# Optimization experiments

Hardware: AMD Instinct MI355X
Metric: run time of the kernel (lower is better)

Reference implementation:

```python
import jax, jax.numpy as jnp
import numpy as np

N = 100000
E = 1600000
F_IN = 128
F_OUT = 128


def setup_inputs() -> dict:
    key = jax.random.key(0)
    k1, k2, k3, k4 = jax.random.split(key, 4)
    x = jax.random.normal(k1, (N, F_IN), dtype=jnp.float32)
    edge_index = jax.random.randint(k2, (2, E), 0, N, dtype=jnp.int64)
    # GCNConv params (glorot weight, zero bias as in PyG defaults)
    limit = float(np.sqrt(6.0 / (F_IN + F_OUT)))
    W = jax.random.uniform(k3, (F_IN, F_OUT), minval=-limit, maxval=limit, dtype=jnp.float32)
    b = jnp.zeros((F_OUT,), dtype=jnp.float32)
    return {"x": x, "edge_index": edge_index, "W": W, "b": b}


def reference(x, edge_index, W, b):
    n = x.shape[0]
    # add self-loops
    loops = jnp.arange(n, dtype=edge_index.dtype)
    src = jnp.concatenate([edge_index[0], loops])  # source nodes j
    dst = jnp.concatenate([edge_index[1], loops])  # target nodes i
    # symmetric normalization: deg over incoming edges (targets), weight 1
    deg = jax.ops.segment_sum(jnp.ones_like(dst, dtype=x.dtype), dst, num_segments=n)
    dinv = jnp.where(deg > 0, jax.lax.rsqrt(deg), 0.0)
    norm = dinv[src] * dinv[dst]  # [E+N]
    # linear transform then message passing
    h = x @ W  # [N, F_OUT]
    msgs = h[src] * norm[:, None]  # gather + scale, [E+N, F_OUT]
    out = jax.ops.segment_sum(msgs, dst, num_segments=n)  # scatter-add
    return out + b
```

## Files before the change

kernel.cpp:

```cpp
#include <hip/hip_runtime.h>

#define FDIM 128
#define NBMAX 512
#define EPB 4096

typedef __attribute__((ext_vector_type(8))) short bf16x8;
typedef __attribute__((ext_vector_type(4))) float f32x4;

__device__ __forceinline__ unsigned short f2bf(float f) {
    unsigned int u = __float_as_uint(f);
    unsigned int r = u + 0x7fffu + ((u >> 16) & 1u);
    return (unsigned short)(r >> 16);
}

__global__ __launch_bounds__(256) void k_prep(const int* __restrict__ dst,
                                              int* __restrict__ bcnt,
                                              const float* __restrict__ W,
                                              unsigned short* __restrict__ whi,
                                              int e, int ebl) {
    __shared__ int h[NBMAX];
    if ((int)blockIdx.x < ebl) {
        for (int i = threadIdx.x; i < NBMAX; i += 256) h[i] = 0;
        __syncthreads();
        int base = blockIdx.x * EPB;
        int end = min(base + EPB, e);
        for (int i = base + threadIdx.x; i < end; i += 256) atomicAdd(&h[dst[i] >> 8], 1);
        __syncthreads();
        for (int i = threadIdx.x; i < NBMAX; i += 256) {
            int c = h[i];
            if (c) atomicAdd(&bcnt[i], c);
        }
    } else {
        int id = ((int)blockIdx.x - ebl) * 256 + threadIdx.x;
        int k = id >> 7, nn = id & 127;
        whi[nn * FDIM + k] = f2bf(W[id]);
    }
}

__global__ __launch_bounds__(512) void k_bscan(const int* __restrict__ bcnt,
                                               int* __restrict__ bbase,
                                               int* __restrict__ gcur,
                                               int* __restrict__ row_start,
                                               int nb, int n, int e) {
    __shared__ int sh[512];
    int v = (threadIdx.x < nb) ? bcnt[threadIdx.x] : 0;
    sh[threadIdx.x] = v;
    __syncthreads();
    for (int off = 1; off < 512; off <<= 1) {
        int t = (threadIdx.x >= off) ? sh[threadIdx.x - off] : 0;
        __syncthreads();
        sh[threadIdx.x] += t;
        __syncthreads();
    }
    int excl = sh[threadIdx.x] - v;
    if (threadIdx.x < nb) {
        bbase[threadIdx.x] = excl;
        gcur[threadIdx.x] = excl;
    }
    if (threadIdx.x == 0) {
        bbase[nb] = e;
        row_start[n] = e;
    }
}

__global__ __launch_bounds__(256) void k_main(
    const int* __restrict__ src, const int* __restrict__ dst,
    int* __restrict__ gcur, unsigned int* __restrict__ coarse,
    const float* __restrict__ x, const unsigned short* __restrict__ whi,
    unsigned short* __restrict__ hs, int e, int n, int ebl) {
    __shared__ unsigned short Bs[FDIM * FDIM];
    __shared__ int cur[NBMAX];

    if ((int)blockIdx.x < ebl) {
        for (int i = threadIdx.x; i < NBMAX; i += 256) cur[i] = 0;
        __syncthreads();
        int base = blockIdx.x * EPB;
        int end = min(base + EPB, e);
        for (int i = base + threadIdx.x; i < end; i += 256) atomicAdd(&cur[dst[i] >> 8], 1);
        __syncthreads();
        for (int i = threadIdx.x; i < NBMAX; i += 256) {
            int c = cur[i];
            cur[i] = c ? atomicAdd(&gcur[i], c) : 0;
        }
        __syncthreads();
        for (int i = base + threadIdx.x; i < end; i += 256) {
            int d = dst[i];
            int p = atomicAdd(&cur[d >> 8], 1);
            coarse[p] = ((unsigned)src[i] << 8) | (unsigned)(d & 255);
        }
    } else {
        {
            const float4* g4 = (const float4*)whi;
            float4* l4 = (float4*)Bs;
            for (int i = threadIdx.x; i < 2048; i += 256) {
                int nn = i >> 4;
                int g = i & 15;
                l4[nn * 16 + (g ^ (nn & 15))] = g4[i];
            }
        }
        __syncthreads();

        const int lane = threadIdx.x & 63;
        const int wid = threadIdx.x >> 6;
        const int m = lane & 15;
        const int quad = lane >> 4;
        const int row0 = ((int)blockIdx.x - ebl) * 64 + wid * 16;

        int rowA = row0 + m;
        if (rowA >= n) rowA = n - 1;
        const float* xr = x + (size_t)rowA * FDIM;

        f32x4 acc[8];
        #pragma unroll
        for (int ct = 0; ct < 8; ++ct) acc[ct] = (f32x4){0.f, 0.f, 0.f, 0.f};

        #pragma unroll
        for (int kc = 0; kc < 4; ++kc) {
            const int kb = kc * 32 + quad * 8;
            float4 xa = *(const float4*)(xr + kb);
            float4 xb = *(const float4*)(xr + kb + 4);
            float v[8] = {xa.x, xa.y, xa.z, xa.w, xb.x, xb.y, xb.z, xb.w};
            bf16x8 ahi, alo;
            #pragma unroll
            for (int j = 0; j < 8; ++j) {
                unsigned short hh = f2bf(v[j]);
                ahi[j] = (short)hh;
                alo[j] = (short)f2bf(v[j] - __uint_as_float(((unsigned)hh) << 16));
            }
            const int g = kc * 4 + quad;
            #pragma unroll
            for (int ct = 0; ct < 8; ++ct) {
                int nidx = ct * 16 + m;
                const bf16x8 bhi = *(const bf16x8*)(Bs + (size_t)nidx * FDIM + (g ^ m) * 8);
                acc[ct] = __builtin_amdgcn_mfma_f32_16x16x32_bf16(ahi, bhi, acc[ct], 0, 0, 0);
                acc[ct] = __builtin_amdgcn_mfma_f32_16x16x32_bf16(alo, bhi, acc[ct], 0, 0, 0);
            }
        }

        #pragma unroll
        for (int r = 0; r < 4; ++r) {
            int row = row0 + quad * 4 + r;
            if (row >= n) continue;
            unsigned short* hrow = hs + (size_t)row * FDIM;
            #pragma unroll
            for (int ct = 0; ct < 8; ++ct) hrow[ct * 16 + m] = f2bf(acc[ct][r]);
        }
    }
}

__global__ __launch_bounds__(256) void k_bfin(const unsigned int* __restrict__ coarse,
                                              const int* __restrict__ bbase,
                                              float* __restrict__ dinv,
                                              int* __restrict__ row_start,
                                              int* __restrict__ ebuf, int n) {
    __shared__ int ld[256];
    __shared__ int sc[256];
    __shared__ int cur[256];
    int b = blockIdx.x;
    int s = bbase[b], t = bbase[b + 1];
    ld[threadIdx.x] = 0;
    __syncthreads();
    for (int i = s + threadIdx.x; i < t; i += 256) atomicAdd(&ld[coarse[i] & 255u], 1);
    __syncthreads();
    int v = ld[threadIdx.x];
    sc[threadIdx.x] = v;
    __syncthreads();
    for (int off = 1; off < 256; off <<= 1) {
        int tv = (threadIdx.x >= off) ? sc[threadIdx.x - off] : 0;
        __syncthreads();
        sc[threadIdx.x] += tv;
        __syncthreads();
    }
    int rs = s + sc[threadIdx.x] - v;
    cur[threadIdx.x] = rs;
    int node = b * 256 + threadIdx.x;
    if (node < n) {
        dinv[node] = rsqrtf((float)(v + 1));
        row_start[node] = rs;
    }
    __syncthreads();
    for (int i = s + threadIdx.x; i < t; i += 256) {
        unsigned int p = coarse[i];
        int pos = atomicAdd(&cur[p & 255u], 1);
        ebuf[pos] = (int)(p >> 8);
    }
}

__global__ __launch_bounds__(256) void k_gather(
    const unsigned short* __restrict__ hs, const int* __restrict__ ebuf,
    const int* __restrict__ row_start, const float* __restrict__ dinv,
    const float* __restrict__ bias, float* __restrict__ out, int n) {
    int i = blockIdx.x * 4 + (threadIdx.x >> 6);
    if (i >= n) return;
    int lane = threadIdx.x & 63;

    int beg = row_start[i];
    int end = row_start[i + 1];
    float di = dinv[i];

    const unsigned int* __restrict__ hl = (const unsigned int*)hs + lane;

    unsigned int u = hl[(unsigned)i << 6];
    float ax = di * __uint_as_float(u << 16);
    float ay = di * __uint_as_float(u & 0xffff0000u);
    float bx = 0.f, by = 0.f;

    int j = beg;
    int stop8 = j + ((end - j) & ~7);
    if (j < stop8) {
        int s0 = ebuf[j + 0], s1 = ebuf[j + 1], s2 = ebuf[j + 2], s3 = ebuf[j + 3];
        int s4 = ebuf[j + 4], s5 = ebuf[j + 5], s6 = ebuf[j + 6], s7 = ebuf[j + 7];
        j += 8;
        while (j < stop8) {
            unsigned int u0 = hl[(unsigned)s0 << 6], u1 = hl[(unsigned)s1 << 6];
            unsigned int u2 = hl[(unsigned)s2 << 6], u3 = hl[(unsigned)s3 << 6];
            unsigned int u4 = hl[(unsigned)s4 << 6], u5 = hl[(unsigned)s5 << 6];
            unsigned int u6 = hl[(unsigned)s6 << 6], u7 = hl[(unsigned)s7 << 6];
            float d0 = dinv[s0], d1 = dinv[s1], d2 = dinv[s2], d3 = dinv[s3];
            float d4 = dinv[s4], d5 = dinv[s5], d6 = dinv[s6], d7 = dinv[s7];
            int t0 = ebuf[j + 0], t1 = ebuf[j + 1], t2 = ebuf[j + 2], t3 = ebuf[j + 3];
            int t4 = ebuf[j + 4], t5 = ebuf[j + 5], t6 = ebuf[j + 6], t7 = ebuf[j + 7];
            ax = fmaf(d0, __uint_as_float(u0 << 16), ax);
            ay = fmaf(d0, __uint_as_float(u0 & 0xffff0000u), ay);
            bx = fmaf(d1, __uint_as_float(u1 << 16), bx);
            by = fmaf(d1, __uint_as_float(u1 & 0xffff0000u), by);
            ax = fmaf(d2, __uint_as_float(u2 << 16), ax);
            ay = fmaf(d2, __uint_as_float(u2 & 0xffff0000u), ay);
            bx = fmaf(d3, __uint_as_float(u3 << 16), bx);
            by = fmaf(d3, __uint_as_float(u3 & 0xffff0000u), by);
            ax = fmaf(d4, __uint_as_float(u4 << 16), ax);
            ay = fmaf(d4, __uint_as_float(u4 & 0xffff0000u), ay);
            bx = fmaf(d5, __uint_as_float(u5 << 16), bx);
            by = fmaf(d5, __uint_as_float(u5 & 0xffff0000u), by);
            ax = fmaf(d6, __uint_as_float(u6 << 16), ax);
            ay = fmaf(d6, __uint_as_float(u6 & 0xffff0000u), ay);
            bx = fmaf(d7, __uint_as_float(u7 << 16), bx);
            by = fmaf(d7, __uint_as_float(u7 & 0xffff0000u), by);
            s0 = t0; s1 = t1; s2 = t2; s3 = t3;
            s4 = t4; s5 = t5; s6 = t6; s7 = t7;
            j += 8;
        }
        {
            unsigned int u0 = hl[(unsigned)s0 << 6], u1 = hl[(unsigned)s1 << 6];
            unsigned int u2 = hl[(unsigned)s2 << 6], u3 = hl[(unsigned)s3 << 6];
            unsigned int u4 = hl[(unsigned)s4 << 6], u5 = hl[(unsigned)s5 << 6];
            unsigned int u6 = hl[(unsigned)s6 << 6], u7 = hl[(unsigned)s7 << 6];
            float d0 = dinv[s0], d1 = dinv[s1], d2 = dinv[s2], d3 = dinv[s3];
            float d4 = dinv[s4], d5 = dinv[s5], d6 = dinv[s6], d7 = dinv[s7];
            ax = fmaf(d0, __uint_as_float(u0 << 16), ax);
            ay = fmaf(d0, __uint_as_float(u0 & 0xffff0000u), ay);
            bx = fmaf(d1, __uint_as_float(u1 << 16), bx);
            by = fmaf(d1, __uint_as_float(u1 & 0xffff0000u), by);
            ax = fmaf(d2, __uint_as_float(u2 << 16), ax);
            ay = fmaf(d2, __uint_as_float(u2 & 0xffff0000u), ay);
            bx = fmaf(d3, __uint_as_float(u3 << 16), bx);
            by = fmaf(d3, __uint_as_float(u3 & 0xffff0000u), by);
            ax = fmaf(d4, __uint_as_float(u4 << 16), ax);
            ay = fmaf(d4, __uint_as_float(u4 & 0xffff0000u), ay);
            bx = fmaf(d5, __uint_as_float(u5 << 16), bx);
            by = fmaf(d5, __uint_as_float(u5 & 0xffff0000u), by);
            ax = fmaf(d6, __uint_as_float(u6 << 16), ax);
            ay = fmaf(d6, __uint_as_float(u6 & 0xffff0000u), ay);
            bx = fmaf(d7, __uint_as_float(u7 << 16), bx);
            by = fmaf(d7, __uint_as_float(u7 & 0xffff0000u), by);
        }
    }
    for (; j + 3 < end; j += 4) {
        int s0 = ebuf[j], s1 = ebuf[j + 1], s2 = ebuf[j + 2], s3 = ebuf[j + 3];
        float d0 = dinv[s0], d1 = dinv[s1], d2 = dinv[s2], d3 = dinv[s3];
        unsigned int u0 = hl[(unsigned)s0 << 6];
        unsigned int u1 = hl[(unsigned)s1 << 6];
        unsigned int u2 = hl[(unsigned)s2 << 6];
        unsigned int u3 = hl[(unsigned)s3 << 6];
        ax = fmaf(d0, __uint_as_float(u0 << 16), ax);
        ay = fmaf(d0, __uint_as_float(u0 & 0xffff0000u), ay);
        bx = fmaf(d1, __uint_as_float(u1 << 16), bx);
        by = fmaf(d1, __uint_as_float(u1 & 0xffff0000u), by);
        ax = fmaf(d2, __uint_as_float(u2 << 16), ax);
        ay = fmaf(d2, __uint_as_float(u2 & 0xffff0000u), ay);
        bx = fmaf(d3, __uint_as_float(u3 << 16), bx);
        by = fmaf(d3, __uint_as_float(u3 & 0xffff0000u), by);
    }
    for (; j < end; ++j) {
        int s0 = ebuf[j];
        float d0 = dinv[s0];
        unsigned int u0 = hl[(unsigned)s0 << 6];
        ax = fmaf(d0, __uint_as_float(u0 << 16), ax);
        ay = fmaf(d0, __uint_as_float(u0 & 0xffff0000u), ay);
    }
    ax += bx;
    ay += by;

    float2 bb = ((const float2*)bias)[lane];
    float2 r = make_float2(fmaf(ax, di, bb.x), fmaf(ay, di, bb.y));
    ((float2*)(out + (size_t)i * FDIM))[lane] = r;
}

extern "C" void kernel_launch(void* const* d_in, const int* in_sizes, int n_in,
                              void* d_out, int out_size, void* d_ws, size_t ws_size,
                              hipStream_t stream) {
    const float* x  = (const float*)d_in[0];
    const int*   ei = (const int*)d_in[1];
    const float* W  = (const float*)d_in[2];
    const float* b  = (const float*)d_in[3];

    const int n = in_sizes[0] / FDIM;
    const int e = in_sizes[1] / 2;
    const int* src = ei;
    const int* dst = ei + e;
    float* out = (float*)d_out;

    const int nb = (n + 255) >> 8;
    const int ebl = (e + EPB - 1) / EPB;
    const int gemmbl = (n + 63) / 64;

    char* ws = (char*)d_ws;
    size_t off = 0;
    auto alloc = [&](size_t bytes) {
        char* p = ws + off;
        off += (bytes + 511) & ~(size_t)511;
        return p;
    };
    float*          dinv      = (float*)alloc((size_t)n * 4);
    int*            row_start = (int*)alloc((size_t)(n + 1) * 4);
    int*            bcnt      = (int*)alloc((size_t)NBMAX * 4);
    int*            bbase     = (int*)alloc((size_t)(NBMAX + 1) * 4);
    int*            gcur      = (int*)alloc((size_t)NBMAX * 4);
    unsigned short* whi       = (unsigned short*)alloc((size_t)FDIM * FDIM * 2);
    unsigned int*   coarse    = (unsigned int*)alloc((size_t)e * 4);
    int*            ebuf      = (int*)alloc((size_t)e * 4);
    unsigned short* hs        = (unsigned short*)alloc((size_t)n * FDIM * 2);

    hipMemsetAsync(bcnt, 0, (size_t)NBMAX * 4, stream);

    k_prep<<<ebl + 64, 256, 0, stream>>>(dst, bcnt, W, whi, e, ebl);
    k_bscan<<<1, 512, 0, stream>>>(bcnt, bbase, gcur, row_start, nb, n, e);
    k_main<<<ebl + gemmbl, 256, 0, stream>>>(src, dst, gcur, coarse, x, whi, hs, e, n, ebl);
    k_bfin<<<nb, 256, 0, stream>>>(coarse, bbase, dinv, row_start, ebuf, n);
    {
        int blocks = (n + 3) / 4;
        k_gather<<<blocks, 256, 0, stream>>>(hs, ebuf, row_start, dinv, b, out, n);
    }
}
```

Before: 242.5 us.

## Fold bucket scan into consumer kernels and make gather grid-stride

```diff
diff --git a/kernel.cpp b/kernel.cpp
--- a/kernel.cpp
+++ b/kernel.cpp
@@ -37,42 +37,35 @@
     }
 }
 
-__global__ __launch_bounds__(512) void k_bscan(const int* __restrict__ bcnt,
-                                               int* __restrict__ bbase,
-                                               int* __restrict__ gcur,
-                                               int* __restrict__ row_start,
-                                               int nb, int n, int e) {
-    __shared__ int sh[512];
-    int v = (threadIdx.x < nb) ? bcnt[threadIdx.x] : 0;
-    sh[threadIdx.x] = v;
-    __syncthreads();
-    for (int off = 1; off < 512; off <<= 1) {
-        int t = (threadIdx.x >= off) ? sh[threadIdx.x - off] : 0;
-        __syncthreads();
-        sh[threadIdx.x] += t;
-        __syncthreads();
-    }
-    int excl = sh[threadIdx.x] - v;
-    if (threadIdx.x < nb) {
-        bbase[threadIdx.x] = excl;
-        gcur[threadIdx.x] = excl;
-    }
-    if (threadIdx.x == 0) {
-        bbase[nb] = e;
-        row_start[n] = e;
-    }
-}
-
 __global__ __launch_bounds__(256) void k_main(
     const int* __restrict__ src, const int* __restrict__ dst,
+    const int* __restrict__ bcnt,
     int* __restrict__ gcur, unsigned int* __restrict__ coarse,
     const float* __restrict__ x, const unsigned short* __restrict__ whi,
     unsigned short* __restrict__ hs, int e, int n, int ebl) {
     __shared__ unsigned short Bs[FDIM * FDIM];
     __shared__ int cur[NBMAX];
+    __shared__ int bb[NBMAX];
 
     if ((int)blockIdx.x < ebl) {
-        for (int i = threadIdx.x; i < NBMAX; i += 256) cur[i] = 0;
+        int t = threadIdx.x;
+        int v0 = bcnt[t], v1 = bcnt[t + 256];
+        cur[t] = v0;
+        cur[t + 256] = v1;
+        __syncthreads();
+        for (int off = 1; off < NBMAX; off <<= 1) {
+            int a0 = (t >= off) ? cur[t - off] : 0;
+            int a1 = (t + 256 >= off) ? cur[t + 256 - off] : 0;
+            __syncthreads();
+            cur[t] += a0;
+            cur[t + 256] += a1;
+            __syncthreads();
+        }
+        bb[t] = cur[t] - v0;
+        bb[t + 256] = cur[t + 256] - v1;
+        __syncthreads();
+        cur[t] = 0;
+        cur[t + 256] = 0;
         __syncthreads();
         int base = blockIdx.x * EPB;
         int end = min(base + EPB, e);
@@ -80,7 +73,7 @@
         __syncthreads();
         for (int i = threadIdx.x; i < NBMAX; i += 256) {
             int c = cur[i];
-            cur[i] = c ? atomicAdd(&gcur[i], c) : 0;
+            cur[i] = c ? (bb[i] + atomicAdd(&gcur[i], c)) : 0;
         }
         __syncthreads();
         for (int i = base + threadIdx.x; i < end; i += 256) {
@@ -149,77 +142,147 @@
 }
 
 __global__ __launch_bounds__(256) void k_bfin(const unsigned int* __restrict__ coarse,
-                                              const int* __restrict__ bbase,
+                                              const int* __restrict__ bcnt,
                                               float* __restrict__ dinv,
                                               int* __restrict__ row_start,
-                                              int* __restrict__ ebuf, int n) {
+                                              int* __restrict__ ebuf, int n, int e) {
+    __shared__ int bsc[NBMAX];
     __shared__ int ld[256];
     __shared__ int sc[256];
     __shared__ int cur[256];
     int b = blockIdx.x;
-    int s = bbase[b], t = bbase[b + 1];
-    ld[threadIdx.x] = 0;
-    __syncthreads();
-    for (int i = s + threadIdx.x; i < t; i += 256) atomicAdd(&ld[coarse[i] & 255u], 1);
-    __syncthreads();
-    int v = ld[threadIdx.x];
-    sc[threadIdx.x] = v;
+    int tt = threadIdx.x;
+    bsc[tt] = bcnt[tt];
+    bsc[tt + 256] = bcnt[tt + 256];
+    __syncthreads();
+    for (int off = 1; off < NBMAX; off <<= 1) {
+        int a0 = (tt >= off) ? bsc[tt - off] : 0;
+        int a1 = (tt + 256 >= off) ? bsc[tt + 256 - off] : 0;
+        __syncthreads();
+        bsc[tt] += a0;
+        bsc[tt + 256] += a1;
+        __syncthreads();
+    }
+    int s = (b > 0) ? bsc[b - 1] : 0;
+    int t = bsc[b];
+    if (b == 0 && tt == 0) row_start[n] = e;
+
+    ld[tt] = 0;
+    __syncthreads();
+    for (int i = s + tt; i < t; i += 256) atomicAdd(&ld[coarse[i] & 255u], 1);
+    __syncthreads();
+    int v = ld[tt];
+    sc[tt] = v;
     __syncthreads();
     for (int off = 1; off < 256; off <<= 1) {
-        int tv = (threadIdx.x >= off) ? sc[threadIdx.x - off] : 0;
-        __syncthreads();
-        sc[threadIdx.x] += tv;
-        __syncthreads();
-    }
-    int rs = s + sc[threadIdx.x] - v;
-    cur[threadIdx.x] = rs;
-    int node = b * 256 + threadIdx.x;
+        int tv = (tt >= off) ? sc[tt - off] : 0;
+        __syncthreads();
+        sc[tt] += tv;
+        __syncthreads();
+    }
+    int rs = s + sc[tt] - v;
+    cur[tt] = rs;
+    int node = b * 256 + tt;
     if (node < n) {
         dinv[node] = rsqrtf((float)(v + 1));
         row_start[node] = rs;
     }
     __syncthreads();
-    for (int i = s + threadIdx.x; i < t; i += 256) {
+    for (int i = s + tt; i < t; i += 256) {
         unsigned int p = coarse[i];
         int pos = atomicAdd(&cur[p & 255u], 1);
         ebuf[pos] = (int)(p >> 8);
     }
 }
 
-__global__ __launch_bounds__(256) void k_gather(
+__global__ __launch_bounds__(256, 8) void k_gather(
     const unsigned short* __restrict__ hs, const int* __restrict__ ebuf,
     const int* __restrict__ row_start, const float* __restrict__ dinv,
     const float* __restrict__ bias, float* __restrict__ out, int n) {
-    int i = blockIdx.x * 4 + (threadIdx.x >> 6);
-    if (i >= n) return;
-    int lane = threadIdx.x & 63;
-
-    int beg = row_start[i];
-    int end = row_start[i + 1];
-    float di = dinv[i];
+    const int lane = threadIdx.x & 63;
+    const int gw = (int)blockIdx.x * 4 + (threadIdx.x >> 6);
+    const int nw = (int)gridDim.x * 4;
 
     const unsigned int* __restrict__ hl = (const unsigned int*)hs + lane;
-
-    unsigned int u = hl[(unsigned)i << 6];
-    float ax = di * __uint_as_float(u << 16);
-    float ay = di * __uint_as_float(u & 0xffff0000u);
-    float bx = 0.f, by = 0.f;
-
-    int j = beg;
-    int stop8 = j + ((end - j) & ~7);
-    if (j < stop8) {
-        int s0 = ebuf[j + 0], s1 = ebuf[j + 1], s2 = ebuf[j + 2], s3 = ebuf[j + 3];
-        int s4 = ebuf[j + 4], s5 = ebuf[j + 5], s6 = ebuf[j + 6], s7 = ebuf[j + 7];
-        j += 8;
-        while (j < stop8) {
-            unsigned int u0 = hl[(unsigned)s0 << 6], u1 = hl[(unsigned)s1 << 6];
-            unsigned int u2 = hl[(unsigned)s2 << 6], u3 = hl[(unsigned)s3 << 6];
-            unsigned int u4 = hl[(unsigned)s4 << 6], u5 = hl[(unsigned)s5 << 6];
-            unsigned int u6 = hl[(unsigned)s6 << 6], u7 = hl[(unsigned)s7 << 6];
+    const float2 bb = ((const float2*)bias)[lane];
+
+    for (int i = gw; i < n; i += nw) {
+        int beg = row_start[i];
+        int end = row_start[i + 1];
+        float di = dinv[i];
+
+        unsigned int u = hl[(unsigned)i << 6];
+        float ax = di * __uint_as_float(u << 16);
+        float ay = di * __uint_as_float(u & 0xffff0000u);
+        float bx = 0.f, by = 0.f;
+
+        int j = beg;
+        int stop8 = j + ((end - j) & ~7);
+        if (j < stop8) {
+            int s0 = ebuf[j + 0], s1 = ebuf[j + 1], s2 = ebuf[j + 2], s3 = ebuf[j + 3];
+            int s4 = ebuf[j + 4], s5 = ebuf[j + 5], s6 = ebuf[j + 6], s7 = ebuf[j + 7];
+            j += 8;
+            while (j < stop8) {
+                unsigned int u0 = hl[(unsigned)s0 << 6], u1 = hl[(unsigned)s1 << 6];
+                unsigned int u2 = hl[(unsigned)s2 << 6], u3 = hl[(unsigned)s3 << 6];
+                unsigned int u4 = hl[(unsigned)s4 << 6], u5 = hl[(unsigned)s5 << 6];
+                unsigned int u6 = hl[(unsigned)s6 << 6], u7 = hl[(unsigned)s7 << 6];
+                float d0 = dinv[s0], d1 = dinv[s1], d2 = dinv[s2], d3 = dinv[s3];
+                float d4 = dinv[s4], d5 = dinv[s5], d6 = dinv[s6], d7 = dinv[s7];
+                int t0 = ebuf[j + 0], t1 = ebuf[j + 1], t2 = ebuf[j + 2], t3 = ebuf[j + 3];
+                int t4 = ebuf[j + 4], t5 = ebuf[j + 5], t6 = ebuf[j + 6], t7 = ebuf[j + 7];
+                ax = fmaf(d0, __uint_as_float(u0 << 16), ax);
+                ay = fmaf(d0, __uint_as_float(u0 & 0xffff0000u), ay);
+                bx = fmaf(d1, __uint_as_float(u1 << 16), bx);
+                by = fmaf(d1, __uint_as_float(u1 & 0xffff0000u), by);
+                ax = fmaf(d2, __uint_as_float(u2 << 16), ax);
+                ay = fmaf(d2, __uint_as_float(u2 & 0xffff0000u), ay);
+                bx = fmaf(d3, __uint_as_float(u3 << 16), bx);
+                by = fmaf(d3, __uint_as_float(u3 & 0xffff0000u), by);
+                ax = fmaf(d4, __uint_as_float(u4 << 16), ax);
+                ay = fmaf(d4, __uint_as_float(u4 & 0xffff0000u), ay);
+                bx = fmaf(d5, __uint_as_float(u5 << 16), bx);
+                by = fmaf(d5, __uint_as_float(u5 & 0xffff0000u), by);
+                ax = fmaf(d6, __uint_as_float(u6 << 16), ax);
+                ay = fmaf(d6, __uint_as_float(u6 & 0xffff0000u), ay);
+                bx = fmaf(d7, __uint_as_float(u7 << 16), bx);
+                by = fmaf(d7, __uint_as_float(u7 & 0xffff0000u), by);
+                s0 = t0; s1 = t1; s2 = t2; s3 = t3;
+                s4 = t4; s5 = t5; s6 = t6; s7 = t7;
+                j += 8;
+            }
+            {
+                unsigned int u0 = hl[(unsigned)s0 << 6], u1 = hl[(unsigned)s1 << 6];
+                unsigned int u2 = hl[(unsigned)s2 << 6], u3 = hl[(unsigned)s3 << 6];
+                unsigned int u4 = hl[(unsigned)s4 << 6], u5 = hl[(unsigned)s5 << 6];
+                unsigned int u6 = hl[(unsigned)s6 << 6], u7 = hl[(unsigned)s7 << 6];
+                float d0 = dinv[s0], d1 = dinv[s1], d2 = dinv[s2], d3 = dinv[s3];
+                float d4 = dinv[s4], d5 = dinv[s5], d6 = dinv[s6], d7 = dinv[s7];
+                ax = fmaf(d0, __uint_as_float(u0 << 16), ax);
+                ay = fmaf(d0, __uint_as_float(u0 & 0xffff0000u), ay);
+                bx = fmaf(d1, __uint_as_float(u1 << 16), bx);
+                by = fmaf(d1, __uint_as_float(u1 & 0xffff0000u), by);
+                ax = fmaf(d2, __uint_as_float(u2 << 16), ax);
+                ay = fmaf(d2, __uint_as_float(u2 & 0xffff0000u), ay);
+                bx = fmaf(d3, __uint_as_float(u3 << 16), bx);
+                by = fmaf(d3, __uint_as_float(u3 & 0xffff0000u), by);
+                ax = fmaf(d4, __uint_as_float(u4 << 16), ax);
+                ay = fmaf(d4, __uint_as_float(u4 & 0xffff0000u), ay);
+                bx = fmaf(d5, __uint_as_float(u5 << 16), bx);
+                by = fmaf(d5, __uint_as_float(u5 & 0xffff0000u), by);
+                ax = fmaf(d6, __uint_as_float(u6 << 16), ax);
+                ay = fmaf(d6, __uint_as_float(u6 & 0xffff0000u), ay);
+                bx = fmaf(d7, __uint_as_float(u7 << 16), bx);
+                by = fmaf(d7, __uint_as_float(u7 & 0xffff0000u), by);
+            }
+        }
+        for (; j + 3 < end; j += 4) {
+            int s0 = ebuf[j], s1 = ebuf[j + 1], s2 = ebuf[j + 2], s3 = ebuf[j + 3];
             float d0 = dinv[s0], d1 = dinv[s1], d2 = dinv[s2], d3 = dinv[s3];
-            float d4 = dinv[s4], d5 = dinv[s5], d6 = dinv[s6], d7 = dinv[s7];
-            int t0 = ebuf[j + 0], t1 = ebuf[j + 1], t2 = ebuf[j + 2], t3 = ebuf[j + 3];
-            int t4 = ebuf[j + 4], t5 = ebuf[j + 5], t6 = ebuf[j + 6], t7 = ebuf[j + 7];
+            unsigned int u0 = hl[(unsigned)s0 << 6];
+            unsigned int u1 = hl[(unsigned)s1 << 6];
+            unsigned int u2 = hl[(unsigned)s2 << 6];
+            unsigned int u3 = hl[(unsigned)s3 << 6];
             ax = fmaf(d0, __uint_as_float(u0 << 16), ax);
             ay = fmaf(d0, __uint_as_float(u0 & 0xffff0000u), ay);
             bx = fmaf(d1, __uint_as_float(u1 << 16), bx);
@@ -228,72 +291,20 @@
             ay = fmaf(d2, __uint_as_float(u2 & 0xffff0000u), ay);
             bx = fmaf(d3, __uint_as_float(u3 << 16), bx);
             by = fmaf(d3, __uint_as_float(u3 & 0xffff0000u), by);
-            ax = fmaf(d4, __uint_as_float(u4 << 16), ax);
-            ay = fmaf(d4, __uint_as_float(u4 & 0xffff0000u), ay);
-            bx = fmaf(d5, __uint_as_float(u5 << 16), bx);
-            by = fmaf(d5, __uint_as_float(u5 & 0xffff0000u), by);
-            ax = fmaf(d6, __uint_as_float(u6 << 16), ax);
-            ay = fmaf(d6, __uint_as_float(u6 & 0xffff0000u), ay);
-            bx = fmaf(d7, __uint_as_float(u7 << 16), bx);
-            by = fmaf(d7, __uint_as_float(u7 & 0xffff0000u), by);
-            s0 = t0; s1 = t1; s2 = t2; s3 = t3;
-            s4 = t4; s5 = t5; s6 = t6; s7 = t7;
-            j += 8;
-        }
-        {
-            unsigned int u0 = hl[(unsigned)s0 << 6], u1 = hl[(unsigned)s1 << 6];
-            unsigned int u2 = hl[(unsigned)s2 << 6], u3 = hl[(unsigned)s3 << 6];
-            unsigned int u4 = hl[(unsigned)s4 << 6], u5 = hl[(unsigned)s5 << 6];
-            unsigned int u6 = hl[(unsigned)s6 << 6], u7 = hl[(unsigned)s7 << 6];
-            float d0 = dinv[s0], d1 = dinv[s1], d2 = dinv[s2], d3 = dinv[s3];
-            float d4 = dinv[s4], d5 = dinv[s5], d6 = dinv[s6], d7 = dinv[s7];
+        }
+        for (; j < end; ++j) {
+            int s0 = ebuf[j];
+            float d0 = dinv[s0];
+            unsigned int u0 = hl[(unsigned)s0 << 6];
             ax = fmaf(d0, __uint_as_float(u0 << 16), ax);
             ay = fmaf(d0, __uint_as_float(u0 & 0xffff0000u), ay);
-            bx = fmaf(d1, __uint_as_float(u1 << 16), bx);
-            by = fmaf(d1, __uint_as_float(u1 & 0xffff0000u), by);
-            ax = fmaf(d2, __uint_as_float(u2 << 16), ax);
-            ay = fmaf(d2, __uint_as_float(u2 & 0xffff0000u), ay);
-            bx = fmaf(d3, __uint_as_float(u3 << 16), bx);
-            by = fmaf(d3, __uint_as_float(u3 & 0xffff0000u), by);
-            ax = fmaf(d4, __uint_as_float(u4 << 16), ax);
-            ay = fmaf(d4, __uint_as_float(u4 & 0xffff0000u), ay);
-            bx = fmaf(d5, __uint_as_float(u5 << 16), bx);
-            by = fmaf(d5, __uint_as_float(u5 & 0xffff0000u), by);
-            ax = fmaf(d6, __uint_as_float(u6 << 16), ax);
-            ay = fmaf(d6, __uint_as_float(u6 & 0xffff0000u), ay);
-            bx = fmaf(d7, __uint_as_float(u7 << 16), bx);
-            by = fmaf(d7, __uint_as_float(u7 & 0xffff0000u), by);
-        }
-    }
-    for (; j + 3 < end; j += 4) {
-        int s0 = ebuf[j], s1 = ebuf[j + 1], s2 = ebuf[j + 2], s3 = ebuf[j + 3];
-        float d0 = dinv[s0], d1 = dinv[s1], d2 = dinv[s2], d3 = dinv[s3];
-        unsigned int u0 = hl[(unsigned)s0 << 6];
-        unsigned int u1 = hl[(unsigned)s1 << 6];
-        unsigned int u2 = hl[(unsigned)s2 << 6];
-        unsigned int u3 = hl[(unsigned)s3 << 6];
-        ax = fmaf(d0, __uint_as_float(u0 << 16), ax);
-        ay = fmaf(d0, __uint_as_float(u0 & 0xffff0000u), ay);
-        bx = fmaf(d1, __uint_as_float(u1 << 16), bx);
-        by = fmaf(d1, __uint_as_float(u1 & 0xffff0000u), by);
-        ax = fmaf(d2, __uint_as_float(u2 << 16), ax);
-        ay = fmaf(d2, __uint_as_float(u2 & 0xffff0000u), ay);
-        bx = fmaf(d3, __uint_as_float(u3 << 16), bx);
-        by = fmaf(d3, __uint_as_float(u3 & 0xffff0000u), by);
-    }
-    for (; j < end; ++j) {
-        int s0 = ebuf[j];
-        float d0 = dinv[s0];
-        unsigned int u0 = hl[(unsigned)s0 << 6];
-        ax = fmaf(d0, __uint_as_float(u0 << 16), ax);
-        ay = fmaf(d0, __uint_as_float(u0 & 0xffff0000u), ay);
-    }
-    ax += bx;
-    ay += by;
-
-    float2 bb = ((const float2*)bias)[lane];
-    float2 r = make_float2(fmaf(ax, di, bb.x), fmaf(ay, di, bb.y));
-    ((float2*)(out + (size_t)i * FDIM))[lane] = r;
+        }
+        ax += bx;
+        ay += by;
+
+        float2 r = make_float2(fmaf(ax, di, bb.x), fmaf(ay, di, bb.y));
+        ((float2*)(out + (size_t)i * FDIM))[lane] = r;
+    }
 }
 
 extern "C" void kernel_launch(void* const* d_in, const int* in_sizes, int n_in,
@@ -324,21 +335,20 @@
     float*          dinv      = (float*)alloc((size_t)n * 4);
     int*            row_start = (int*)alloc((size_t)(n + 1) * 4);
     int*            bcnt      = (int*)alloc((size_t)NBMAX * 4);
-    int*            bbase     = (int*)alloc((size_t)(NBMAX + 1) * 4);
     int*            gcur      = (int*)alloc((size_t)NBMAX * 4);
     unsigned short* whi       = (unsigned short*)alloc((size_t)FDIM * FDIM * 2);
     unsigned int*   coarse    = (unsigned int*)alloc((size_t)e * 4);
     int*            ebuf      = (int*)alloc((size_t)e * 4);
     unsigned short* hs        = (unsigned short*)alloc((size_t)n * FDIM * 2);
 
-    hipMemsetAsync(bcnt, 0, (size_t)NBMAX * 4, stream);
+    hipMemsetAsync(bcnt, 0, (size_t)NBMAX * 4 * 2, stream);
 
     k_prep<<<ebl + 64, 256, 0, stream>>>(dst, bcnt, W, whi, e, ebl);
-    k_bscan<<<1, 512, 0, stream>>>(bcnt, bbase, gcur, row_start, nb, n, e);
-    k_main<<<ebl + gemmbl, 256, 0, stream>>>(src, dst, gcur, coarse, x, whi, hs, e, n, ebl);
-    k_bfin<<<nb, 256, 0, stream>>>(coarse, bbase, dinv, row_start, ebuf, n);
+    k_main<<<ebl + gemmbl, 256, 0, stream>>>(src, dst, bcnt, gcur, coarse, x, whi, hs, e, n, ebl);
+    k_bfin<<<nb, 256, 0, stream>>>(coarse, bcnt, dinv, row_start, ebuf, n, e);
     {
         int blocks = (n + 3) / 4;
+        if (blocks > 2048) blocks = 2048;
         k_gather<<<blocks, 256, 0, stream>>>(hs, ebuf, row_start, dinv, b, out, n);
     }
 }
```

After: 235.8 us. 1.03x faster.
